# Performance work log

Measured on AMD Instinct MI355X. Metric: run time of the kernel, lower is better.

## Reference

```python
import jax, jax.numpy as jnp
import numpy as np

N, KS, C = 1_000_000, 9, 16
EPS = 1e-5
SLOPE = 0.2  # LeakyReLU negative_slope


def _leaky(x):
    return jnp.where(x >= 0, x, SLOPE * x)


def _batchnorm(x, gamma, beta):
    # BatchNorm1d in training mode: biased batch statistics over the N axis
    mean = x.mean(axis=0)
    var = x.var(axis=0)
    return gamma * (x - mean) * jax.lax.rsqrt(var + EPS) + beta


def setup_inputs() -> dict:
    key = jax.random.key(0)
    k = jax.random.split(key, 5)
    xav = (2.0 / (C + C)) ** 0.5  # xavier-normal-ish scale for [C_in, C_out, ks]
    return {
        "data": jax.random.normal(k[0], (N, C), jnp.float32),
        "ind": jax.random.randint(k[1], (N, KS), 0, N),
        "w1": jax.random.normal(k[2], (C, C, KS), jnp.float32) * xav,
        "b1": jax.random.normal(k[3], (C,), jnp.float32) * 0.01,
        "gamma1": jnp.ones((C,), jnp.float32),
        "beta1": jnp.zeros((C,), jnp.float32),
        "w2": jax.random.normal(k[4], (C, C, KS), jnp.float32) * xav,
        "gamma2": jnp.ones((C,), jnp.float32),
        "beta2": jnp.zeros((C,), jnp.float32),
    }


def reference(data, ind, w1, b1, gamma1, beta1, w2, gamma2, beta2):
    # gather neighborhoods: [N, ks, C]
    inp = data[ind]
    # torch.einsum('ijk,klj->il', data[N,ks,C], weight[C,Cout,ks]) -> [N, Cout]
    out = jnp.einsum('njc,coj->no', inp, w1) + b1
    out = _leaky(_batchnorm(out, gamma1, beta1))
    # second gather + tree-conv, no bias
    out = jnp.einsum('njc,coj->no', out[ind], w2)
    out = _batchnorm(out, gamma2, beta2)
    # residual (in_channels == out_channels -> identity shortcut)
    return _leaky(out + data)
```

## Files before the change

### kernel.cpp

```cpp
#include <hip/hip_runtime.h>

typedef unsigned int uint;
typedef unsigned short ushort;

#define NN 1000000
#define KSZ 9
#define CH 16
#define KTOT 144
#define LSTR 168
#define NBLK 1024
#define TILES64 15625

typedef float f32x4 __attribute__((ext_vector_type(4)));
typedef short s16x8 __attribute__((ext_vector_type(8)));

__device__ __forceinline__ float bf2f(ushort v) { return __uint_as_float(((uint)v) << 16); }
__device__ __forceinline__ ushort f2bf(float f) {
  uint u = __float_as_uint(f);
  return (ushort)((u + 0x7fffu + ((u >> 16) & 1u)) >> 16);
}
__device__ __forceinline__ float leaky(float x) { return x >= 0.f ? x : 0.2f * x; }

template<bool FP32SRC>
__global__ __launch_bounds__(256)
void k_conv(const void* __restrict__ srcv, const int* __restrict__ ind,
            const float* __restrict__ w, const float* __restrict__ bias,
            const float* __restrict__ derived, ushort* __restrict__ outv,
            float* __restrict__ partial) {
  const int lane = threadIdx.x & 63;
  const int wid  = threadIdx.x >> 6;
  const int o = lane & 15;
  const int q = lane >> 4;

  __shared__ ushort lds[4][16 * LSTR];
  __shared__ float red[4][32];
  ushort* my = lds[wid];

  {
    int n = lane >> 2, part = lane & 3;
    *(unsigned long long*)&my[n * LSTR + KTOT + part * 4] = 0ULL;
  }

  s16x8 bfrag[5];
#pragma unroll
  for (int t = 0; t < 5; ++t) {
#pragma unroll
    for (int i = 0; i < 8; ++i) {
      int k = t * 32 + q * 8 + i;
      ushort wv = 0;
      if (k < KTOT) { int j = k >> 4, c = k & 15; wv = f2bf(w[(c * CH + o) * KSZ + j]); }
      bfrag[t][i] = (short)wv;
    }
  }

  float bo = FP32SRC ? bias[o] : 0.f;

  float sc[16], sh[16];
  if (!FP32SRC) {
#pragma unroll
    for (int b = 0; b < 4; ++b) {
      float4 v = *(const float4*)(derived + b * 4);
      sc[b*4+0]=v.x; sc[b*4+1]=v.y; sc[b*4+2]=v.z; sc[b*4+3]=v.w;
      float4 u = *(const float4*)(derived + 16 + b * 4);
      sh[b*4+0]=u.x; sh[b*4+1]=u.y; sh[b*4+2]=u.z; sh[b*4+3]=u.w;
    }
  }

  float wsum = 0.f, wsq = 0.f;

  for (int g = blockIdx.x; g < TILES64; g += NBLK) {
    const int base = g * 64 + wid * 16;

    int idxv[3];
#pragma unroll
    for (int ph = 0; ph < 3; ++ph) {
      int r = lane + ph * 64;
      int rr = (r < KTOT) ? r : lane;
      int nsub = rr / KSZ;
      int j = rr - nsub * KSZ;
      idxv[ph] = ind[(base + nsub) * KSZ + j];
    }

#pragma unroll
    for (int ph = 0; ph < 3; ++ph) {
      int r = lane + ph * 64;
      if (r < KTOT) {
        int nsub = r / KSZ;
        int j = r - nsub * KSZ;
        int idx = idxv[ph];
        uint pk[8];
        if (FP32SRC) {
          const float4* sp = (const float4*)((const float*)srcv + (size_t)idx * CH);
          float4 f0 = sp[0], f1 = sp[1], f2 = sp[2], f3 = sp[3];
          float e[16] = {f0.x,f0.y,f0.z,f0.w, f1.x,f1.y,f1.z,f1.w,
                         f2.x,f2.y,f2.z,f2.w, f3.x,f3.y,f3.z,f3.w};
#pragma unroll
          for (int p = 0; p < 8; ++p)
            pk[p] = (uint)f2bf(e[2*p]) | ((uint)f2bf(e[2*p+1]) << 16);
        } else {
          const uint4* s4 = (const uint4*)((const ushort*)srcv + (size_t)idx * CH);
          uint4 lo = s4[0], hi = s4[1];
          uint uu[8] = {lo.x, lo.y, lo.z, lo.w, hi.x, hi.y, hi.z, hi.w};
#pragma unroll
          for (int p = 0; p < 8; ++p) {
            float e0 = __uint_as_float(uu[p] << 16);
            float e1 = __uint_as_float(uu[p] & 0xffff0000u);
            float x0 = leaky(sc[2*p] * e0 + sh[2*p]);
            float x1 = leaky(sc[2*p+1] * e1 + sh[2*p+1]);
            pk[p] = (uint)f2bf(x0) | ((uint)f2bf(x1) << 16);
          }
        }
        uint4* d4 = (uint4*)&my[nsub * LSTR + j * CH];
        d4[0] = *(uint4*)&pk[0];
        d4[1] = *(uint4*)&pk[4];
      }
    }

    const ushort* ap = &my[o * LSTR + q * 8];
    f32x4 acc = {0.f, 0.f, 0.f, 0.f};
#pragma unroll
    for (int t = 0; t < 5; ++t) {
      s16x8 a = *(const s16x8*)(ap + t * 32);
      acc = __builtin_amdgcn_mfma_f32_16x16x32_bf16(a, bfrag[t], acc, 0, 0, 0);
    }
#pragma unroll
    for (int r = 0; r < 4; ++r) {
      float v = acc[r] + bo;
      ushort hv = f2bf(v);
      outv[(size_t)(base + q * 4 + r) * CH + o] = hv;
      float vr = bf2f(hv);
      wsum += vr;
      wsq  += vr * vr;
    }
  }

  wsum += __shfl_xor(wsum, 16);  wsum += __shfl_xor(wsum, 32);
  wsq  += __shfl_xor(wsq, 16);   wsq  += __shfl_xor(wsq, 32);
  if (lane < 16) { red[wid][lane] = wsum; red[wid][16 + lane] = wsq; }
  __syncthreads();
  if (threadIdx.x < 32) {
    float s = red[0][threadIdx.x] + red[1][threadIdx.x] + red[2][threadIdx.x] + red[3][threadIdx.x];
    partial[blockIdx.x * 32 + threadIdx.x] = s;
  }
}

__global__ __launch_bounds__(1024)
void k_finalize(const float* __restrict__ partial, const float* __restrict__ gamma,
                const float* __restrict__ beta, float* __restrict__ derived) {
  __shared__ float red[32][33];
  __shared__ float tot[32];
  int t = threadIdx.x, ch = t & 31, seg = t >> 5;
  float s = 0.f;
#pragma unroll
  for (int i = 0; i < 32; i += 8) {
    float a0 = partial[(seg * 32 + i + 0) * 32 + ch];
    float a1 = partial[(seg * 32 + i + 1) * 32 + ch];
    float a2 = partial[(seg * 32 + i + 2) * 32 + ch];
    float a3 = partial[(seg * 32 + i + 3) * 32 + ch];
    float a4 = partial[(seg * 32 + i + 4) * 32 + ch];
    float a5 = partial[(seg * 32 + i + 5) * 32 + ch];
    float a6 = partial[(seg * 32 + i + 6) * 32 + ch];
    float a7 = partial[(seg * 32 + i + 7) * 32 + ch];
    s += ((a0 + a1) + (a2 + a3)) + ((a4 + a5) + (a6 + a7));
  }
  red[seg][ch] = s;
  __syncthreads();
  if (t < 32) {
    float x = 0.f;
#pragma unroll
    for (int k = 0; k < 32; ++k) x += red[k][t];
    tot[t] = x;
  }
  __syncthreads();
  if (t < 16) {
    float mean = tot[t] * (1.0f / NN);
    float var  = tot[16 + t] * (1.0f / NN) - mean * mean;
    float scale = gamma[t] / sqrtf(var + 1e-5f);
    derived[t] = scale;
    derived[16 + t] = beta[t] - mean * scale;
  }
}

__global__ __launch_bounds__(256)
void k_final(const ushort* __restrict__ o2, const float* __restrict__ data,
             const float* __restrict__ drv, float* __restrict__ out) {
  size_t t = (size_t)blockIdx.x * 256 + threadIdx.x;
  size_t i0 = t * 8;
  if (i0 >= (size_t)NN * CH) return;
  int coff = (int)(i0 & 15);
  float4 s0 = *(const float4*)(drv + coff);
  float4 s1 = *(const float4*)(drv + coff + 4);
  float4 h0 = *(const float4*)(drv + 16 + coff);
  float4 h1 = *(const float4*)(drv + 16 + coff + 4);
  float sc[8] = {s0.x,s0.y,s0.z,s0.w,s1.x,s1.y,s1.z,s1.w};
  float sh[8] = {h0.x,h0.y,h0.z,h0.w,h1.x,h1.y,h1.z,h1.w};
  uint4 a = *(const uint4*)(o2 + i0);
  float4 d0 = *(const float4*)(data + i0);
  float4 d1 = *(const float4*)(data + i0 + 4);
  uint ua[4] = {a.x,a.y,a.z,a.w};
  float dd[8] = {d0.x,d0.y,d0.z,d0.w, d1.x,d1.y,d1.z,d1.w};
  float y[8];
#pragma unroll
  for (int p = 0; p < 4; ++p) {
    float x0 = __uint_as_float(ua[p] << 16);
    float x1 = __uint_as_float(ua[p] & 0xffff0000u);
    y[2*p]   = leaky(sc[2*p]   * x0 + sh[2*p]   + dd[2*p]);
    y[2*p+1] = leaky(sc[2*p+1] * x1 + sh[2*p+1] + dd[2*p+1]);
  }
  float4 r0 = {y[0], y[1], y[2], y[3]};
  float4 r1 = {y[4], y[5], y[6], y[7]};
  *(float4*)(out + i0) = r0;
  *(float4*)(out + i0 + 4) = r1;
}

extern "C" void kernel_launch(void* const* d_in, const int* in_sizes, int n_in,
                              void* d_out, int out_size, void* d_ws, size_t ws_size,
                              hipStream_t stream) {
  const float* data   = (const float*)d_in[0];
  const int*   ind    = (const int*)d_in[1];
  const float* w1     = (const float*)d_in[2];
  const float* b1     = (const float*)d_in[3];
  const float* gamma1 = (const float*)d_in[4];
  const float* beta1  = (const float*)d_in[5];
  const float* w2     = (const float*)d_in[6];
  const float* gamma2 = (const float*)d_in[7];
  const float* beta2  = (const float*)d_in[8];
  float* out = (float*)d_out;

  ushort* out1 = (ushort*)d_out;
  ushort* out2     = (ushort*)d_ws;
  float*  partial1 = (float*)((char*)d_ws + 32000000);
  float*  partial2 = partial1 + NBLK * 32;
  float*  derived1 = partial2 + NBLK * 32;
  float*  derived2 = derived1 + 32;

  hipLaunchKernelGGL((k_conv<true>), dim3(NBLK), dim3(256), 0, stream,
                     (const void*)data, ind, w1, b1, (const float*)nullptr, out1, partial1);
  hipLaunchKernelGGL(k_finalize, dim3(1), dim3(1024), 0, stream,
                     partial1, gamma1, beta1, derived1);
  hipLaunchKernelGGL((k_conv<false>), dim3(NBLK), dim3(256), 0, stream,
                     (const void*)out1, ind, w2, (const float*)nullptr, derived1, out2, partial2);
  hipLaunchKernelGGL(k_finalize, dim3(1), dim3(1024), 0, stream,
                     partial2, gamma2, beta2, derived2);
  hipLaunchKernelGGL(k_final, dim3((NN * CH / 8 + 255) / 256), dim3(256), 0, stream,
                     out2, data, derived2, out);
}
```

Before: 471.9 us.

## Gather MFMA A-fragments directly from global memory and fold BN finalize into consumers

Adds a pre-pass that casts the fp32 input to bf16, so the first conv gathers 32-byte bf16 rows instead of 64-byte fp32 rows. Each lane now loads its MFMA A-fragment straight from global memory with inline-asm dwordx4 loads, removing the LDS staging of gathered rows. The separate finalize kernels are dropped: per-block statistics are atomically added into a global accumulator, and each consumer kernel computes the BN scale and shift itself. The cost is an extra cast pass, fp32 atomics with nondeterministic summation order, a memset, and a full vmcnt(0) wait after each batch of gathers, which limits overlap between loads and compute.

```diff
diff --git a/kernel.cpp b/kernel.cpp
--- a/kernel.cpp
+++ b/kernel.cpp
@@ -7,7 +7,6 @@
 #define KSZ 9
 #define CH 16
 #define KTOT 144
-#define LSTR 168
 #define NBLK 1024
 #define TILES64 15625
 
@@ -21,25 +20,37 @@
 }
 __device__ __forceinline__ float leaky(float x) { return x >= 0.f ? x : 0.2f * x; }
 
-template<bool FP32SRC>
 __global__ __launch_bounds__(256)
-void k_conv(const void* __restrict__ srcv, const int* __restrict__ ind,
+void k_cast(const float* __restrict__ in, ushort* __restrict__ out) {
+  size_t i0 = ((size_t)blockIdx.x * 256 + (size_t)threadIdx.x) * 8;
+  if (i0 >= (size_t)NN * CH) return;
+  float4 a = *(const float4*)(in + i0);
+  float4 b = *(const float4*)(in + i0 + 4);
+  float e[8] = {a.x, a.y, a.z, a.w, b.x, b.y, b.z, b.w};
+  uint pk[4];
+#pragma unroll
+  for (int p = 0; p < 4; ++p)
+    pk[p] = (uint)f2bf(e[2*p]) | ((uint)f2bf(e[2*p+1]) << 16);
+  *(uint4*)(out + i0) = *(uint4*)pk;
+}
+
+template<bool BN>
+__global__ __launch_bounds__(256)
+void k_conv(const ushort* __restrict__ src, const int* __restrict__ ind,
             const float* __restrict__ w, const float* __restrict__ bias,
-            const float* __restrict__ derived, ushort* __restrict__ outv,
-            float* __restrict__ partial) {
+            const float* __restrict__ statsIn, const float* __restrict__ gamma,
+            const float* __restrict__ beta,
+            ushort* __restrict__ outv, float* __restrict__ accumOut) {
   const int lane = threadIdx.x & 63;
   const int wid  = threadIdx.x >> 6;
   const int o = lane & 15;
   const int q = lane >> 4;
-
-  __shared__ ushort lds[4][16 * LSTR];
+  const int qh = q >> 1;
+  const int ch0 = (q & 1) * 8;
+
+  __shared__ int   idxs[4][160];
   __shared__ float red[4][32];
-  ushort* my = lds[wid];
-
-  {
-    int n = lane >> 2, part = lane & 3;
-    *(unsigned long long*)&my[n * LSTR + KTOT + part * 4] = 0ULL;
-  }
+  __shared__ float dsc[16], dsh[16];
 
   s16x8 bfrag[5];
 #pragma unroll
@@ -53,76 +64,82 @@
     }
   }
 
-  float bo = FP32SRC ? bias[o] : 0.f;
-
-  float sc[16], sh[16];
-  if (!FP32SRC) {
-#pragma unroll
-    for (int b = 0; b < 4; ++b) {
-      float4 v = *(const float4*)(derived + b * 4);
-      sc[b*4+0]=v.x; sc[b*4+1]=v.y; sc[b*4+2]=v.z; sc[b*4+3]=v.w;
-      float4 u = *(const float4*)(derived + 16 + b * 4);
-      sh[b*4+0]=u.x; sh[b*4+1]=u.y; sh[b*4+2]=u.z; sh[b*4+3]=u.w;
-    }
-  }
-
+  float bo = 0.f;
+  float sc8[8], sh8[8];
+  if constexpr (BN) {
+    if (threadIdx.x < 16) {
+      int c = threadIdx.x;
+      float s = statsIn[c], sq = statsIn[16 + c];
+      float mean = s * (1.0f / NN);
+      float var  = sq * (1.0f / NN) - mean * mean;
+      float scale = gamma[c] * rsqrtf(var + 1e-5f);
+      dsc[c] = scale; dsh[c] = beta[c] - mean * scale;
+    }
+    __syncthreads();
+#pragma unroll
+    for (int i = 0; i < 8; ++i) { sc8[i] = dsc[ch0 + i]; sh8[i] = dsh[ch0 + i]; }
+  } else {
+    bo = bias[o];
+  }
+
+  int* idxw = idxs[wid];
   float wsum = 0.f, wsq = 0.f;
 
   for (int g = blockIdx.x; g < TILES64; g += NBLK) {
-    const int base = g * 64 + wid * 16;
-
-    int idxv[3];
-#pragma unroll
-    for (int ph = 0; ph < 3; ++ph) {
-      int r = lane + ph * 64;
-      int rr = (r < KTOT) ? r : lane;
-      int nsub = rr / KSZ;
-      int j = rr - nsub * KSZ;
-      idxv[ph] = ind[(base + nsub) * KSZ + j];
-    }
-
-#pragma unroll
-    for (int ph = 0; ph < 3; ++ph) {
-      int r = lane + ph * 64;
-      if (r < KTOT) {
-        int nsub = r / KSZ;
-        int j = r - nsub * KSZ;
-        int idx = idxv[ph];
-        uint pk[8];
-        if (FP32SRC) {
-          const float4* sp = (const float4*)((const float*)srcv + (size_t)idx * CH);
-          float4 f0 = sp[0], f1 = sp[1], f2 = sp[2], f3 = sp[3];
-          float e[16] = {f0.x,f0.y,f0.z,f0.w, f1.x,f1.y,f1.z,f1.w,
-                         f2.x,f2.y,f2.z,f2.w, f3.x,f3.y,f3.z,f3.w};
-#pragma unroll
-          for (int p = 0; p < 8; ++p)
-            pk[p] = (uint)f2bf(e[2*p]) | ((uint)f2bf(e[2*p+1]) << 16);
-        } else {
-          const uint4* s4 = (const uint4*)((const ushort*)srcv + (size_t)idx * CH);
-          uint4 lo = s4[0], hi = s4[1];
-          uint uu[8] = {lo.x, lo.y, lo.z, lo.w, hi.x, hi.y, hi.z, hi.w};
-#pragma unroll
-          for (int p = 0; p < 8; ++p) {
-            float e0 = __uint_as_float(uu[p] << 16);
-            float e1 = __uint_as_float(uu[p] & 0xffff0000u);
-            float x0 = leaky(sc[2*p] * e0 + sh[2*p]);
-            float x1 = leaky(sc[2*p+1] * e1 + sh[2*p+1]);
-            pk[p] = (uint)f2bf(x0) | ((uint)f2bf(x1) << 16);
-          }
+    const int base  = g * 64 + wid * 16;
+    const int base9 = base * 9;
+
+    {
+      int r = lane;            idxw[r] = ind[base9 + r];
+      r = lane + 64;           idxw[r] = ind[base9 + r];
+      r = lane + 128; if (r < KTOT) idxw[r] = ind[base9 + r];
+    }
+
+    int i0 = idxw[o * KSZ + (0 + qh)];
+    int i1 = idxw[o * KSZ + (2 + qh)];
+    int i2 = idxw[o * KSZ + (4 + qh)];
+    int i3 = idxw[o * KSZ + (6 + qh)];
+    int i4 = idxw[o * KSZ + 8];
+
+    const ushort* p0 = src + (size_t)i0 * CH + ch0;
+    const ushort* p1 = src + (size_t)i1 * CH + ch0;
+    const ushort* p2 = src + (size_t)i2 * CH + ch0;
+    const ushort* p3 = src + (size_t)i3 * CH + ch0;
+    const ushort* p4 = src + (size_t)i4 * CH + ch0;
+
+    s16x8 ld0, ld1, ld2, ld3, ld4;
+    asm volatile("global_load_dwordx4 %0, %1, off sc0" : "=&v"(ld0) : "v"(p0) : "memory");
+    asm volatile("global_load_dwordx4 %0, %1, off sc0" : "=&v"(ld1) : "v"(p1) : "memory");
+    asm volatile("global_load_dwordx4 %0, %1, off sc0" : "=&v"(ld2) : "v"(p2) : "memory");
+    asm volatile("global_load_dwordx4 %0, %1, off sc0" : "=&v"(ld3) : "v"(p3) : "memory");
+    asm volatile("global_load_dwordx4 %0, %1, off sc0" : "=&v"(ld4) : "v"(p4) : "memory");
+    asm volatile("s_waitcnt vmcnt(0)" ::: "memory");
+    __builtin_amdgcn_sched_barrier(0);
+
+    s16x8 a0, a1, a2, a3, a4;
+    if constexpr (BN) {
+      auto xf = [&](s16x8 v) -> s16x8 {
+        s16x8 r;
+#pragma unroll
+        for (int i = 0; i < 8; ++i) {
+          float x = bf2f((ushort)v[i]);
+          r[i] = (short)f2bf(leaky(sc8[i] * x + sh8[i]));
         }
-        uint4* d4 = (uint4*)&my[nsub * LSTR + j * CH];
-        d4[0] = *(uint4*)&pk[0];
-        d4[1] = *(uint4*)&pk[4];
-      }
-    }
-
-    const ushort* ap = &my[o * LSTR + q * 8];
+        return r;
+      };
+      a0 = xf(ld0); a1 = xf(ld1); a2 = xf(ld2); a3 = xf(ld3); a4 = xf(ld4);
+    } else {
+      a0 = ld0; a1 = ld1; a2 = ld2; a3 = ld3; a4 = ld4;
+    }
+    if (qh) { s16x8 z = {0,0,0,0,0,0,0,0}; a4 = z; }
+
     f32x4 acc = {0.f, 0.f, 0.f, 0.f};
-#pragma unroll
-    for (int t = 0; t < 5; ++t) {
-      s16x8 a = *(const s16x8*)(ap + t * 32);
-      acc = __builtin_amdgcn_mfma_f32_16x16x32_bf16(a, bfrag[t], acc, 0, 0, 0);
-    }
+    acc = __builtin_amdgcn_mfma_f32_16x16x32_bf16(a0, bfrag[0], acc, 0, 0, 0);
+    acc = __builtin_amdgcn_mfma_f32_16x16x32_bf16(a1, bfrag[1], acc, 0, 0, 0);
+    acc = __builtin_amdgcn_mfma_f32_16x16x32_bf16(a2, bfrag[2], acc, 0, 0, 0);
+    acc = __builtin_amdgcn_mfma_f32_16x16x32_bf16(a3, bfrag[3], acc, 0, 0, 0);
+    acc = __builtin_amdgcn_mfma_f32_16x16x32_bf16(a4, bfrag[4], acc, 0, 0, 0);
+
 #pragma unroll
     for (int r = 0; r < 4; ++r) {
       float v = acc[r] + bo;
@@ -140,65 +157,36 @@
   __syncthreads();
   if (threadIdx.x < 32) {
     float s = red[0][threadIdx.x] + red[1][threadIdx.x] + red[2][threadIdx.x] + red[3][threadIdx.x];
-    partial[blockIdx.x * 32 + threadIdx.x] = s;
-  }
-}
-
-__global__ __launch_bounds__(1024)
-void k_finalize(const float* __restrict__ partial, const float* __restrict__ gamma,
-                const float* __restrict__ beta, float* __restrict__ derived) {
-  __shared__ float red[32][33];
-  __shared__ float tot[32];
-  int t = threadIdx.x, ch = t & 31, seg = t >> 5;
-  float s = 0.f;
-#pragma unroll
-  for (int i = 0; i < 32; i += 8) {
-    float a0 = partial[(seg * 32 + i + 0) * 32 + ch];
-    float a1 = partial[(seg * 32 + i + 1) * 32 + ch];
-    float a2 = partial[(seg * 32 + i + 2) * 32 + ch];
-    float a3 = partial[(seg * 32 + i + 3) * 32 + ch];
-    float a4 = partial[(seg * 32 + i + 4) * 32 + ch];
-    float a5 = partial[(seg * 32 + i + 5) * 32 + ch];
-    float a6 = partial[(seg * 32 + i + 6) * 32 + ch];
-    float a7 = partial[(seg * 32 + i + 7) * 32 + ch];
-    s += ((a0 + a1) + (a2 + a3)) + ((a4 + a5) + (a6 + a7));
-  }
-  red[seg][ch] = s;
-  __syncthreads();
-  if (t < 32) {
-    float x = 0.f;
-#pragma unroll
-    for (int k = 0; k < 32; ++k) x += red[k][t];
-    tot[t] = x;
-  }
-  __syncthreads();
-  if (t < 16) {
-    float mean = tot[t] * (1.0f / NN);
-    float var  = tot[16 + t] * (1.0f / NN) - mean * mean;
-    float scale = gamma[t] / sqrtf(var + 1e-5f);
-    derived[t] = scale;
-    derived[16 + t] = beta[t] - mean * scale;
+    atomicAdd(&accumOut[threadIdx.x], s);
   }
 }
 
 __global__ __launch_bounds__(256)
 void k_final(const ushort* __restrict__ o2, const float* __restrict__ data,
-             const float* __restrict__ drv, float* __restrict__ out) {
+             const float* __restrict__ statsIn, const float* __restrict__ gamma,
+             const float* __restrict__ beta, float* __restrict__ out) {
+  __shared__ float dsc[16], dsh[16];
+  if (threadIdx.x < 16) {
+    int c = threadIdx.x;
+    float s = statsIn[c], sq = statsIn[16 + c];
+    float mean = s * (1.0f / NN);
+    float var  = sq * (1.0f / NN) - mean * mean;
+    float scale = gamma[c] * rsqrtf(var + 1e-5f);
+    dsc[c] = scale; dsh[c] = beta[c] - mean * scale;
+  }
+  __syncthreads();
   size_t t = (size_t)blockIdx.x * 256 + threadIdx.x;
   size_t i0 = t * 8;
   if (i0 >= (size_t)NN * CH) return;
   int coff = (int)(i0 & 15);
-  float4 s0 = *(const float4*)(drv + coff);
-  float4 s1 = *(const float4*)(drv + coff + 4);
-  float4 h0 = *(const float4*)(drv + 16 + coff);
-  float4 h1 = *(const float4*)(drv + 16 + coff + 4);
-  float sc[8] = {s0.x,s0.y,s0.z,s0.w,s1.x,s1.y,s1.z,s1.w};
-  float sh[8] = {h0.x,h0.y,h0.z,h0.w,h1.x,h1.y,h1.z,h1.w};
+  float sc[8], sh[8];
+#pragma unroll
+  for (int p = 0; p < 8; ++p) { sc[p] = dsc[coff + p]; sh[p] = dsh[coff + p]; }
   uint4 a = *(const uint4*)(o2 + i0);
   float4 d0 = *(const float4*)(data + i0);
   float4 d1 = *(const float4*)(data + i0 + 4);
-  uint ua[4] = {a.x,a.y,a.z,a.w};
-  float dd[8] = {d0.x,d0.y,d0.z,d0.w, d1.x,d1.y,d1.z,d1.w};
+  uint ua[4] = {a.x, a.y, a.z, a.w};
+  float dd[8] = {d0.x, d0.y, d0.z, d0.w, d1.x, d1.y, d1.z, d1.w};
   float y[8];
 #pragma unroll
   for (int p = 0; p < 4; ++p) {
@@ -227,21 +215,24 @@
   const float* beta2  = (const float*)d_in[8];
   float* out = (float*)d_out;
 
-  ushort* out1 = (ushort*)d_out;
-  ushort* out2     = (ushort*)d_ws;
-  float*  partial1 = (float*)((char*)d_ws + 32000000);
-  float*  partial2 = partial1 + NBLK * 32;
-  float*  derived1 = partial2 + NBLK * 32;
-  float*  derived2 = derived1 + 32;
-
+  ushort* out1  = (ushort*)d_out;
+  ushort* dataB = out1 + (size_t)NN * CH;
+  float*  accum1 = (float*)d_ws;
+  float*  accum2 = accum1 + 32;
+  ushort* out2   = (ushort*)((char*)d_ws + 256);
+
+  hipMemsetAsync(d_ws, 0, 256, stream);
+
+  hipLaunchKernelGGL(k_cast, dim3((NN * CH / 8 + 255) / 256), dim3(256), 0, stream,
+                     data, dataB);
+  hipLaunchKernelGGL((k_conv<false>), dim3(NBLK), dim3(256), 0, stream,
+                     dataB, ind, w1, b1,
+                     (const float*)nullptr, (const float*)nullptr, (const float*)nullptr,
+                     out1, accum1);
   hipLaunchKernelGGL((k_conv<true>), dim3(NBLK), dim3(256), 0, stream,
-                     (const void*)data, ind, w1, b1, (const float*)nullptr, out1, partial1);
-  hipLaunchKernelGGL(k_finalize, dim3(1), dim3(1024), 0, stream,
-                     partial1, gamma1, beta1, derived1);
-  hipLaunchKernelGGL((k_conv<false>), dim3(NBLK), dim3(256), 0, stream,
-                     (const void*)out1, ind, w2, (const float*)nullptr, derived1, out2, partial2);
-  hipLaunchKernelGGL(k_finalize, dim3(1), dim3(1024), 0, stream,
-                     partial2, gamma2, beta2, derived2);
+                     out1, ind, w2, (const float*)nullptr,
+                     accum1, gamma1, beta1,
+                     out2, accum2);
   hipLaunchKernelGGL(k_final, dim3((NN * CH / 8 + 255) / 256), dim3(256), 0, stream,
-                     out2, data, derived2, out);
-}
+                     out2, data, accum2, gamma2, beta2, out);
+}
```

New measurement: 471.6 us. About the same (-0.1%).
